# Performance work log

Hardware: AMD Instinct MI355X
Metric: run time of the kernel (lower is better)

Reference implementation:

```python
import jax, jax.numpy as jnp
import numpy as np

# Quantization constants (from init_kwargs)
INPUT_SCALE = 0.05
OUTPUT_SCALE = 0.1
OUTPUT_ZERO_POINT = 0
FEATURE_BITWIDTH = 8
Q_MIN = -(1 << (FEATURE_BITWIDTH - 1))       # -128
Q_MAX = (1 << (FEATURE_BITWIDTH - 1)) - 1    #  127

B, IN_F, OUT_F = 8192, 4096, 4096


def setup_inputs() -> dict:
    key = jax.random.key(0)
    k_x, k_w, k_b, k_s = jax.random.split(key, 4)
    # int8 quantized activations and weights
    x = jax.random.randint(k_x, (B, IN_F), Q_MIN, Q_MAX + 1, dtype=jnp.int8)
    weight = jax.random.randint(k_w, (OUT_F, IN_F), Q_MIN, Q_MAX + 1, dtype=jnp.int8)
    # shifted quantized bias (int32)
    bias = jax.random.randint(k_b, (OUT_F,), -1000, 1000, dtype=jnp.int32)
    # per-output-channel weight scale (positive floats)
    weight_scale = jax.random.uniform(k_s, (OUT_F,), dtype=jnp.float32, minval=0.001, maxval=0.01)
    return {"x": x, "weight": weight, "bias": bias, "weight_scale": weight_scale}


def reference(x, weight, bias, weight_scale):
    # int32-accumulated GEMM: [B, in] @ [in, out] + bias -> [B, out]
    acc = jnp.matmul(x.astype(jnp.int32), weight.astype(jnp.int32).T,
                     preferred_element_type=jnp.int32) + bias[None, :]
    # dequant/requant epilogue with per-channel scale
    out = acc.astype(jnp.float32) * (INPUT_SCALE * weight_scale[None, :] / OUTPUT_SCALE) + OUTPUT_ZERO_POINT
    out = jnp.clip(jnp.round(out), Q_MIN, Q_MAX).astype(jnp.int8)
    return out
```

## Files before the change

### kernel.cpp

```cpp
#include <hip/hip_runtime.h>
#include <cstdint>
#include <cstddef>

#define M_DIM 8192
#define N_DIM 4096
#define K_DIM 4096

#define BM 128
#define BN 128
#define BK 64

using i32x4 = __attribute__((ext_vector_type(4))) int;

__device__ __forceinline__ void async_load16(const void* g, void* l) {
    __builtin_amdgcn_global_load_lds(
        (const __attribute__((address_space(1))) void*)g,
        (__attribute__((address_space(3))) void*)l,
        16, 0, 0);
}

__global__ __launch_bounds__(256) void pack_i8_kernel(const int4* __restrict__ src,
                                                      unsigned* __restrict__ dst,
                                                      long n4) {
    long i = (long)blockIdx.x * blockDim.x + threadIdx.x;
    if (i >= n4) return;
    int4 a = src[i];
    dst[i] = (unsigned)((a.x & 0xff) | ((a.y & 0xff) << 8) |
                        ((a.z & 0xff) << 16) | (a.w << 24));
}

__global__ __launch_bounds__(256) void qgemm_i8_kernel(const int8_t* __restrict__ A,
                                                       const int8_t* __restrict__ B,
                                                       const int* __restrict__ bias,
                                                       const float* __restrict__ wscale,
                                                       int* __restrict__ C) {
    __shared__ int8_t As[BM * BK];
    __shared__ int8_t Bs[BN * BK];

    const int tid  = threadIdx.x;
    const int wave = tid >> 6;
    const int lane = tid & 63;
    const int bm = blockIdx.y;
    const int bn = blockIdx.x;

    const int8_t* Ab = A + (size_t)bm * BM * K_DIM;
    const int8_t* Bb = B + (size_t)bn * BN * K_DIM;

    const int wm = wave >> 1;
    const int wn = wave & 1;

    i32x4 acc[4][4] = {};

    const int srow = lane >> 2;
    const int scol = (lane & 3) * 16;

    const int kq   = (lane >> 4) * 16;
    const int mrow = wm * 64 + (lane & 15);
    const int nrow = wn * 64 + (lane & 15);

    for (int kt = 0; kt < K_DIM; kt += BK) {
#pragma unroll
        for (int c = 0; c < 2; ++c) {
            const int rbase = (c * 4 + wave) * 16;
            async_load16(Ab + (size_t)(rbase + srow) * K_DIM + kt + scol,
                         &As[(c * 4 + wave) * 1024]);
            async_load16(Bb + (size_t)(rbase + srow) * K_DIM + kt + scol,
                         &Bs[(c * 4 + wave) * 1024]);
        }
        __syncthreads();

        i32x4 af[4], bf[4];
#pragma unroll
        for (int i = 0; i < 4; ++i)
            af[i] = *(const i32x4*)&As[(mrow + i * 16) * BK + kq];
#pragma unroll
        for (int j = 0; j < 4; ++j)
            bf[j] = *(const i32x4*)&Bs[(nrow + j * 16) * BK + kq];

#pragma unroll
        for (int i = 0; i < 4; ++i)
#pragma unroll
            for (int j = 0; j < 4; ++j)
                acc[i][j] = __builtin_amdgcn_mfma_i32_16x16x64_i8(af[i], bf[j], acc[i][j], 0, 0, 0);

        __syncthreads();
    }

    const int col16 = lane & 15;
    const int rquad = (lane >> 4) * 4;
#pragma unroll
    for (int j = 0; j < 4; ++j) {
        const int col = bn * BN + wn * 64 + j * 16 + col16;
        float s = 0.05f * wscale[col];
        s = s / 0.1f;
        const float bz = (float)bias[col];
#pragma unroll
        for (int i = 0; i < 4; ++i) {
            const int row0 = bm * BM + wm * 64 + i * 16 + rquad;
#pragma unroll
            for (int r = 0; r < 4; ++r) {
                float v = ((float)acc[i][j][r] + bz) * s;
                v = rintf(v);
                v = fminf(fmaxf(v, -128.0f), 127.0f);
                C[(size_t)(row0 + r) * N_DIM + col] = (int)v;
            }
        }
    }
}

extern "C" void kernel_launch(void* const* d_in, const int* in_sizes, int n_in,
                              void* d_out, int out_size, void* d_ws, size_t ws_size,
                              hipStream_t stream) {
    const int*   x32    = (const int*)d_in[0];
    const int*   w32    = (const int*)d_in[1];
    const int*   bias   = (const int*)d_in[2];
    const float* wscale = (const float*)d_in[3];
    int*         out    = (int*)d_out;

    int8_t* xp = (int8_t*)d_ws;
    int8_t* wp = xp + (size_t)M_DIM * K_DIM;

    {
        long n4 = (long)M_DIM * K_DIM / 4;
        pack_i8_kernel<<<(int)((n4 + 255) / 256), 256, 0, stream>>>(
            (const int4*)x32, (unsigned*)xp, n4);
    }
    {
        long n4 = (long)N_DIM * K_DIM / 4;
        pack_i8_kernel<<<(int)((n4 + 255) / 256), 256, 0, stream>>>(
            (const int4*)w32, (unsigned*)wp, n4);
    }

    dim3 grid(N_DIM / BN, M_DIM / BM);
    qgemm_i8_kernel<<<grid, 256, 0, stream>>>(xp, wp, bias, wscale, out);
}
```

Measured before the change: 421.9 us.

## Switch to 32x32x32 int8 MFMA with XOR-swizzled LDS and fused pack kernel

Replaces the 16x16x64 int8 MFMA tiling with 32x32x32 MFMA instructions using 16-wide accumulators. It XOR-swizzles the LDS chunk placement so fragment reads spread across banks. The two int32-to-int8 pack launches are merged into one kernel to save a launch. The epilogue is remapped to the 32x32 output register layout, which changes the store pattern.

Measured after the change: 429.0 us. No clear change (+1.7%).

```diff
diff --git a/kernel.cpp b/kernel.cpp
--- a/kernel.cpp
+++ b/kernel.cpp
@@ -10,7 +10,8 @@
 #define BN 128
 #define BK 64
 
-using i32x4 = __attribute__((ext_vector_type(4))) int;
+using i32x4  = __attribute__((ext_vector_type(4)))  int;
+using i32x16 = __attribute__((ext_vector_type(16))) int;
 
 __device__ __forceinline__ void async_load16(const void* g, void* l) {
     __builtin_amdgcn_global_load_lds(
@@ -19,14 +20,21 @@
         16, 0, 0);
 }
 
-__global__ __launch_bounds__(256) void pack_i8_kernel(const int4* __restrict__ src,
-                                                      unsigned* __restrict__ dst,
-                                                      long n4) {
+__global__ __launch_bounds__(256) void pack_i8_fused_kernel(const int4* __restrict__ xsrc,
+                                                            const int4* __restrict__ wsrc,
+                                                            unsigned* __restrict__ xdst,
+                                                            unsigned* __restrict__ wdst,
+                                                            long nx4, long ntot4) {
     long i = (long)blockIdx.x * blockDim.x + threadIdx.x;
-    if (i >= n4) return;
-    int4 a = src[i];
-    dst[i] = (unsigned)((a.x & 0xff) | ((a.y & 0xff) << 8) |
-                        ((a.z & 0xff) << 16) | (a.w << 24));
+    if (i >= ntot4) return;
+    const int4* src;
+    unsigned* dst;
+    long si;
+    if (i < nx4) { src = xsrc; dst = xdst; si = i; }
+    else         { src = wsrc; dst = wdst; si = i - nx4; }
+    int4 a = src[si];
+    dst[si] = (unsigned)((a.x & 0xff) | ((a.y & 0xff) << 8) |
+                         ((a.z & 0xff) << 16) | (a.w << 24));
 }
 
 __global__ __launch_bounds__(256) void qgemm_i8_kernel(const int8_t* __restrict__ A,
@@ -49,14 +57,13 @@
     const int wm = wave >> 1;
     const int wn = wave & 1;
 
-    i32x4 acc[4][4] = {};
+    i32x16 acc[2][2] = {};
 
     const int srow = lane >> 2;
-    const int scol = (lane & 3) * 16;
+    const int scol = (((lane & 3) ^ ((srow >> 1) & 3))) * 16;
 
-    const int kq   = (lane >> 4) * 16;
-    const int mrow = wm * 64 + (lane & 15);
-    const int nrow = wn * 64 + (lane & 15);
+    const int l31 = lane & 31;
+    const int khalf = lane >> 5;
 
     for (int kt = 0; kt < K_DIM; kt += BK) {
 #pragma unroll
@@ -69,40 +76,49 @@
         }
         __syncthreads();
 
-        i32x4 af[4], bf[4];
+        i32x4 af[2][2], bf[2][2];
 #pragma unroll
-        for (int i = 0; i < 4; ++i)
-            af[i] = *(const i32x4*)&As[(mrow + i * 16) * BK + kq];
+        for (int t = 0; t < 2; ++t) {
+            const int am = wm * 64 + t * 32 + l31;
+            const int bn_r = wn * 64 + t * 32 + l31;
+            const int aswz = (am >> 1) & 3;
+            const int bswz = (bn_r >> 1) & 3;
 #pragma unroll
-        for (int j = 0; j < 4; ++j)
-            bf[j] = *(const i32x4*)&Bs[(nrow + j * 16) * BK + kq];
+            for (int s = 0; s < 2; ++s) {
+                const int clog = s * 2 + khalf;
+                af[t][s] = *(const i32x4*)&As[am   * BK + ((clog ^ aswz) * 16)];
+                bf[t][s] = *(const i32x4*)&Bs[bn_r * BK + ((clog ^ bswz) * 16)];
+            }
+        }
 
 #pragma unroll
-        for (int i = 0; i < 4; ++i)
+        for (int s = 0; s < 2; ++s)
 #pragma unroll
-            for (int j = 0; j < 4; ++j)
-                acc[i][j] = __builtin_amdgcn_mfma_i32_16x16x64_i8(af[i], bf[j], acc[i][j], 0, 0, 0);
+            for (int ti = 0; ti < 2; ++ti)
+#pragma unroll
+                for (int tj = 0; tj < 2; ++tj)
+                    acc[ti][tj] = __builtin_amdgcn_mfma_i32_32x32x32_i8(
+                        af[ti][s], bf[tj][s], acc[ti][tj], 0, 0, 0);
 
         __syncthreads();
     }
 
-    const int col16 = lane & 15;
-    const int rquad = (lane >> 4) * 4;
 #pragma unroll
-    for (int j = 0; j < 4; ++j) {
-        const int col = bn * BN + wn * 64 + j * 16 + col16;
+    for (int tj = 0; tj < 2; ++tj) {
+        const int col = bn * BN + wn * 64 + tj * 32 + l31;
         float s = 0.05f * wscale[col];
         s = s / 0.1f;
         const float bz = (float)bias[col];
 #pragma unroll
-        for (int i = 0; i < 4; ++i) {
-            const int row0 = bm * BM + wm * 64 + i * 16 + rquad;
+        for (int ti = 0; ti < 2; ++ti) {
+            const int row0 = bm * BM + wm * 64 + ti * 32 + 4 * khalf;
 #pragma unroll
-            for (int r = 0; r < 4; ++r) {
-                float v = ((float)acc[i][j][r] + bz) * s;
+            for (int reg = 0; reg < 16; ++reg) {
+                const int row = row0 + (reg & 3) + 8 * (reg >> 2);
+                float v = ((float)acc[ti][tj][reg] + bz) * s;
                 v = rintf(v);
                 v = fminf(fmaxf(v, -128.0f), 127.0f);
-                C[(size_t)(row0 + r) * N_DIM + col] = (int)v;
+                C[(size_t)row * N_DIM + col] = (int)v;
             }
         }
     }
@@ -121,14 +137,12 @@
     int8_t* wp = xp + (size_t)M_DIM * K_DIM;
 
     {
-        long n4 = (long)M_DIM * K_DIM / 4;
-        pack_i8_kernel<<<(int)((n4 + 255) / 256), 256, 0, stream>>>(
-            (const int4*)x32, (unsigned*)xp, n4);
-    }
-    {
-        long n4 = (long)N_DIM * K_DIM / 4;
-        pack_i8_kernel<<<(int)((n4 + 255) / 256), 256, 0, stream>>>(
-            (const int4*)w32, (unsigned*)wp, n4);
+        long nx4   = (long)M_DIM * K_DIM / 4;
+        long nw4   = (long)N_DIM * K_DIM / 4;
+        long ntot4 = nx4 + nw4;
+        pack_i8_fused_kernel<<<(int)((ntot4 + 255) / 256), 256, 0, stream>>>(
+            (const int4*)x32, (const int4*)w32,
+            (unsigned*)xp, (unsigned*)wp, nx4, ntot4);
     }
 
     dim3 grid(N_DIM / BN, M_DIM / BM);
```
